# Optimization experiments

Hardware: AMD Instinct MI355X
Metric: run time of the kernel (lower is better)

Reference implementation:

```python
import jax, jax.numpy as jnp
import numpy as np

H_SIZE = 1024
N_HEADS = 16
HEAD_DIM = H_SIZE // N_HEADS
TAU2 = 1.0
LN_EPS = 1e-5


def setup_inputs() -> dict:
    key = jax.random.key(0)
    ks = jax.random.split(key, 12)
    B, S = 2, 1024
    s = 1.0 / np.sqrt(H_SIZE)
    inp = {
        "input": jax.random.normal(ks[0], (B, S, H_SIZE), dtype=jnp.float32),
        "input_mask": jnp.ones((B, S), dtype=jnp.float32),
        # uniform(0,1) noise; converted to Gumbel(0,1) inside reference
        "gumbel": jax.random.uniform(ks[1], (B, N_HEADS, S, S), dtype=jnp.float32,
                                     minval=1e-10, maxval=1.0),
        "Wq": jax.random.normal(ks[2], (H_SIZE, H_SIZE), dtype=jnp.float32) * s,
        "bq": jnp.zeros((H_SIZE,), dtype=jnp.float32),
        "Wk": jax.random.normal(ks[3], (H_SIZE, H_SIZE), dtype=jnp.float32) * s,
        "bk": jnp.zeros((H_SIZE,), dtype=jnp.float32),
        "Wv": jax.random.normal(ks[4], (H_SIZE, H_SIZE), dtype=jnp.float32) * s,
        "bv": jnp.zeros((H_SIZE,), dtype=jnp.float32),
        "Wo": jax.random.normal(ks[5], (H_SIZE, H_SIZE), dtype=jnp.float32) * s,
        "bo": jnp.zeros((H_SIZE,), dtype=jnp.float32),
        "gamma": jnp.ones((H_SIZE,), dtype=jnp.float32),
        "beta": jnp.zeros((H_SIZE,), dtype=jnp.float32),
    }
    return inp


def reference(input, input_mask, gumbel, Wq, bq, Wk, bk, Wv, bv, Wo, bo, gamma, beta):
    B, S, _ = input.shape
    # projections -> [B, H, S, D]
    def proj(W, b):
        y = jnp.einsum('bsh,oh->bso', input, W) + b  # torch Linear: x @ W.T + b
        return y.reshape(B, S, N_HEADS, HEAD_DIM).transpose(0, 2, 1, 3)
    qq = proj(Wq, bq)
    kk = proj(Wk, bk)
    vv = proj(Wv, bv)
    # raw scores (NOTE: original has no 1/sqrt(d) scaling)
    interact = jnp.einsum('bhqd,bhkd->bhqk', qq, kk)
    # gumbel-softmax (soft): softmax((logits + g)/tau)
    g = -jnp.log(-jnp.log(gumbel))
    sto_attn = jax.nn.softmax((interact + g) / TAU2, axis=-1)
    # masking: mask_1 over query dim, mask_2 over key dim
    mask = input_mask[:, None, :, None] * input_mask[:, None, None, :]  # [B,1,S,S]
    attn = sto_attn * mask
    # (dropout p=0 -> identity)
    out = jnp.einsum('bhqk,bhkd->bhqd', attn, vv)
    out = out.transpose(0, 2, 1, 3).reshape(B, S, H_SIZE)
    out = jnp.einsum('bsh,oh->bso', out, Wo) + bo
    # residual + layernorm
    x = out + input
    mu = jnp.mean(x, axis=-1, keepdims=True)
    var = jnp.mean(jnp.square(x - mu), axis=-1, keepdims=True)
    return (x - mu) * jax.lax.rsqrt(var + LN_EPS) * gamma + beta
```

## Files before the change

### kernel.cpp

```cpp
#include <hip/hip_runtime.h>

#define S_LEN 1024
#define HSZ   1024
#define NHEAD 16
#define HD    64
#define BATCH 2
#define MROWS 2048
#define SOFTMAX_M0 50.0f

typedef unsigned short u16;
typedef __attribute__((ext_vector_type(8))) short short8;
typedef __attribute__((ext_vector_type(4))) short short4v;
typedef __attribute__((ext_vector_type(4))) float f32x4;

#define MFMA_BF16(a, b, c) __builtin_amdgcn_mfma_f32_16x16x32_bf16((a), (b), (c), 0, 0, 0)

__device__ __forceinline__ u16 f2bf(float f) {
    union { float f; unsigned u; } c; c.f = f;
    unsigned u = c.u;
    u += 0x7fffu + ((u >> 16) & 1u);
    return (u16)(u >> 16);
}
__device__ __forceinline__ float bf2f(u16 s) {
    union { unsigned u; float f; } c; c.u = ((unsigned)s) << 16;
    return c.f;
}
__device__ __forceinline__ short8 ld8(const u16* p) {
    return *reinterpret_cast<const short8*>(p);
}
__device__ __forceinline__ void gld16(const u16* g, u16* l) {
    __builtin_amdgcn_global_load_lds(
        (const __attribute__((address_space(1))) unsigned int*)g,
        (__attribute__((address_space(3))) unsigned int*)l, 16, 0, 0);
}
__device__ __forceinline__ int frag_off(int row, int cbb) {
    return (((row << 3) | (cbb ^ (row & 7))) << 3);
}

template<int MT>
__device__ __forceinline__ void gemm_tile(const u16* __restrict__ Ag,
                                          const u16* __restrict__ Bg,
                                          int klen, u16* As, u16* Bs,
                                          f32x4 (&acc)[MT][4]) {
    const int tid  = threadIdx.x;
    const int wave = tid >> 6, lane = tid & 63;
    const int lr = lane & 15, grp = lane >> 4;
    const int wm = wave >> 1, wn = wave & 1;

#pragma unroll
    for (int mt = 0; mt < MT; mt++)
#pragma unroll
        for (int nt = 0; nt < 4; nt++)
            acc[mt][nt] = (f32x4){0.f, 0.f, 0.f, 0.f};

    for (int k0 = 0; k0 < klen; k0 += 64) {
        __syncthreads();
#pragma unroll
        for (int j = 0; j < MT; j++) {
            int c = j * 256 + tid, row = c >> 3, cb = (c & 7) ^ (row & 7);
            gld16(Ag + (size_t)row * HSZ + k0 + cb * 8, As + c * 8);
        }
#pragma unroll
        for (int j = 0; j < 4; j++) {
            int c = j * 256 + tid, row = c >> 3, cb = (c & 7) ^ (row & 7);
            gld16(Bg + (size_t)row * HSZ + k0 + cb * 8, Bs + c * 8);
        }
        __syncthreads();

#pragma unroll
        for (int h = 0; h < 2; h++) {
            const int cbb = h * 4 + grp;
            short8 af[MT], bf[4];
#pragma unroll
            for (int mt = 0; mt < MT; mt++)
                af[mt] = ld8(As + frag_off(wm * (MT * 16) + mt * 16 + lr, cbb));
#pragma unroll
            for (int nt = 0; nt < 4; nt++)
                bf[nt] = ld8(Bs + frag_off(wn * 64 + nt * 16 + lr, cbb));
#pragma unroll
            for (int mt = 0; mt < MT; mt++)
#pragma unroll
                for (int nt = 0; nt < 4; nt++)
                    acc[mt][nt] = MFMA_BF16(af[mt], bf[nt], acc[mt][nt]);
        }
    }
}

__global__ __launch_bounds__(256)
void convert_kernel(const float* __restrict__ x,  const float* __restrict__ wq,
                    const float* __restrict__ wk, const float* __restrict__ wv,
                    const float* __restrict__ wo, u16* __restrict__ dst) {
    const int XV = (MROWS * HSZ) / 4;
    const int WV = (HSZ * HSZ) / 4;
    int vid = blockIdx.x * 256 + threadIdx.x;
    const float* src; int off;
    if (vid < XV)            { src = x;  off = vid; }
    else if (vid < XV + WV)  { src = wq; off = vid - XV; }
    else if (vid < XV + 2*WV){ src = wk; off = vid - XV - WV; }
    else if (vid < XV + 3*WV){ src = wv; off = vid - XV - 2*WV; }
    else                     { src = wo; off = vid - XV - 3*WV; }
    float4 v = reinterpret_cast<const float4*>(src)[off];
    ushort4 o;
    o.x = f2bf(v.x); o.y = f2bf(v.y); o.z = f2bf(v.z); o.w = f2bf(v.w);
    reinterpret_cast<ushort4*>(dst)[vid] = o;
}

__global__ __launch_bounds__(256)
void qkv_gemm(const u16* __restrict__ xb,
              const u16* __restrict__ wqb, const u16* __restrict__ wkb,
              const u16* __restrict__ wvb,
              const float* __restrict__ bq, const float* __restrict__ bk,
              const float* __restrict__ bv, const float* __restrict__ mask,
              u16* __restrict__ qout, u16* __restrict__ kout,
              u16* __restrict__ vtout) {
    __shared__ u16 As[64 * 64];
    __shared__ u16 Bs[128 * 64];
    const int ntile = blockIdx.x;
    const int mtile = blockIdx.y;
    const int p  = ntile >> 3;
    const int m0 = mtile * 64;
    const int nw = (ntile & 7) * 128;
    const u16*  W    = (p == 0) ? wqb : (p == 1) ? wkb : wvb;
    const float* bias = (p == 0) ? bq : (p == 1) ? bk : bv;

    f32x4 acc[2][4];
    gemm_tile<2>(xb + (size_t)m0 * HSZ, W + (size_t)nw * HSZ, HSZ, As, Bs, acc);

    const int wave = threadIdx.x >> 6, lane = threadIdx.x & 63;
    const int lr = lane & 15, grp = lane >> 4;
    const int wm = wave >> 1, wn = wave & 1;
#pragma unroll
    for (int mt = 0; mt < 2; mt++)
#pragma unroll
        for (int nt = 0; nt < 4; nt++)
#pragma unroll
            for (int r = 0; r < 4; r++) {
                int m = m0 + wm * 32 + mt * 16 + grp * 4 + r;
                int o = nw + wn * 64 + nt * 16 + lr;
                float val = acc[mt][nt][r] + bias[o];
                int b = m >> 10, s = m & 1023, hh = o >> 6, d = o & 63;
                if (p == 0)
                    qout[(((size_t)(b * NHEAD + hh)) * S_LEN + s) * HD + d] = f2bf(val);
                else if (p == 1)
                    kout[(((size_t)(b * NHEAD + hh)) * S_LEN + s) * HD + d] = f2bf(val);
                else
                    vtout[(((size_t)(b * NHEAD + hh)) * HD + d) * S_LEN + s] =
                        f2bf(val * mask[m]);
            }
}

__global__ __launch_bounds__(256, 4)
void attn_kernel(const u16* __restrict__ qb, const u16* __restrict__ kb,
                 const u16* __restrict__ vt, const float* __restrict__ gumbel,
                 u16* __restrict__ po, float* __restrict__ pl) {
    const int bh   = blockIdx.y;
    const int qt   = blockIdx.x;
    const int half = blockIdx.z;
    const int q0 = qt * 64, kbase = half * 512;
    const int tid = threadIdx.x;
    const int wave = tid >> 6, lane = tid & 63;
    const int lr = lane & 15, grp = lane >> 4;

    const u16* Q = qb + (size_t)bh * S_LEN * HD;
    const u16* K = kb + (size_t)bh * S_LEN * HD;
    const u16* V = vt + (size_t)bh * HD * S_LEN;
    const int qw = q0 + wave * 16;
    const float* Gp = gumbel + (size_t)bh * S_LEN * S_LEN + (size_t)(qw + lr) * S_LEN;

    __shared__ u16 Ks[64 * 64];
    __shared__ u16 Vs[64 * 64];
    __shared__ u16 pbuf[4 * 16 * 68];
    u16* pw = pbuf + wave * (16 * 68);

    short8 aq0 = ld8(Q + (size_t)(qw + lr) * HD + grp * 8);
    short8 aq1 = ld8(Q + (size_t)(qw + lr) * HD + 32 + grp * 8);

    f32x4 acco[4];
#pragma unroll
    for (int i = 0; i < 4; i++) acco[i] = (f32x4){0.f, 0.f, 0.f, 0.f};
    float lsum = 0.f;

    f32x4 gc[4], gn[4];
#pragma unroll
    for (int kt = 0; kt < 4; kt++)
        gc[kt] = *reinterpret_cast<const f32x4*>(Gp + kbase + kt * 16 + grp * 4);

#pragma unroll 1
    for (int it = 0; it < 8; it++) {
        const int k0 = kbase + it * 64;

        __syncthreads();
#pragma unroll
        for (int j = 0; j < 2; j++) {
            int c = j * 256 + tid, row = c >> 3, cb = (c & 7) ^ (row & 7);
            gld16(K + (size_t)(k0 + row) * HD + cb * 8, Ks + c * 8);
        }
#pragma unroll
        for (int j = 0; j < 2; j++) {
            int c = j * 256 + tid, row = c >> 3, cb = (c & 7) ^ (row & 7);
            gld16(V + (size_t)row * S_LEN + k0 + cb * 8, Vs + c * 8);
        }
        __syncthreads();

        if (it < 7) {
#pragma unroll
            for (int kt = 0; kt < 4; kt++)
                gn[kt] = *reinterpret_cast<const f32x4*>(
                             Gp + k0 + 64 + kt * 16 + grp * 4);
        }

#pragma unroll
        for (int kt = 0; kt < 4; kt++) {
            short8 kf0 = ld8(Ks + frag_off(kt * 16 + lr, grp));
            short8 kf1 = ld8(Ks + frag_off(kt * 16 + lr, 4 + grp));
            f32x4 a = (f32x4){0.f, 0.f, 0.f, 0.f};
            a = MFMA_BF16(kf0, aq0, a);
            a = MFMA_BF16(kf1, aq1, a);
            float p[4];
#pragma unroll
            for (int r = 0; r < 4; r++) {
                float w = -__builtin_amdgcn_rcpf(__logf(gc[kt][r]));
                p[r] = __expf(a[r] - SOFTMAX_M0) * w;
                lsum += p[r];
            }
            ushort4 pk;
            pk.x = f2bf(p[0]); pk.y = f2bf(p[1]);
            pk.z = f2bf(p[2]); pk.w = f2bf(p[3]);
            *reinterpret_cast<ushort4*>(pw + lr * 68 + kt * 16 + grp * 4) = pk;
        }

        short8 pa[2];
#pragma unroll
        for (int ks = 0; ks < 2; ks++) {
            const u16* pp = pw + lr * 68 + ks * 32 + grp * 8;
            short4v lo = *reinterpret_cast<const short4v*>(pp);
            short4v hi = *reinterpret_cast<const short4v*>(pp + 4);
            pa[ks] = __builtin_shufflevector(lo, hi, 0, 1, 2, 3, 4, 5, 6, 7);
        }

#pragma unroll
        for (int nt = 0; nt < 4; nt++)
#pragma unroll
            for (int ks = 0; ks < 2; ks++)
                acco[nt] = MFMA_BF16(pa[ks],
                                     ld8(Vs + frag_off(nt * 16 + lr, ks * 4 + grp)),
                                     acco[nt]);

        if (it < 7) {
#pragma unroll
            for (int kt = 0; kt < 4; kt++) gc[kt] = gn[kt];
        }
    }

    lsum += __shfl_xor(lsum, 16, 64);
    lsum += __shfl_xor(lsum, 32, 64);

    const int qbase = ((half * 32 + bh) * 16 + qt) * 64 + wave * 16;
    if (lane < 16) pl[qbase + lane] = lsum;

    const int qidx = qbase + grp * 4;
#pragma unroll
    for (int nt = 0; nt < 4; nt++)
#pragma unroll
        for (int r = 0; r < 4; r++)
            po[(size_t)(qidx + r) * 64 + nt * 16 + lr] = f2bf(acco[nt][r]);
}

__global__ __launch_bounds__(256)
void combine_kernel(const u16* __restrict__ po, const float* __restrict__ pl,
                    const float* __restrict__ mask, u16* __restrict__ ctx) {
    const int qt = blockIdx.x, bh = blockIdx.y;
    const int b = bh >> 4, h = bh & 15;
    const int q = threadIdx.x >> 2;
    const int dc = (threadIdx.x & 3) * 16;
    const int i0 = ((0 * 32 + bh) * 16 + qt) * 64 + q;
    const int i1 = ((1 * 32 + bh) * 16 + qt) * 64 + q;
    float l = pl[i0] + pl[i1];
    float mq = mask[b * S_LEN + qt * 64 + q] / l;
    u16* dst = ctx + ((size_t)(b * S_LEN + qt * 64 + q)) * HSZ + h * 64 + dc;
#pragma unroll
    for (int c = 0; c < 2; c++) {
        short8 a = ld8(po + (size_t)i0 * 64 + dc + c * 8);
        short8 bm = ld8(po + (size_t)i1 * 64 + dc + c * 8);
        short8 o;
#pragma unroll
        for (int j = 0; j < 8; j++)
            o[j] = (short)f2bf((bf2f((u16)a[j]) + bf2f((u16)bm[j])) * mq);
        *reinterpret_cast<short8*>(dst + c * 8) = o;
    }
}

__global__ __launch_bounds__(256)
void oproj_gemm(const u16* __restrict__ A, const u16* __restrict__ W,
                float* __restrict__ part0, float* __restrict__ part1) {
    __shared__ u16 As[64 * 64];
    __shared__ u16 Bs[128 * 64];
    const int ntile = blockIdx.x;
    const int mtile = blockIdx.y;
    const int z     = blockIdx.z;
    const int m0 = mtile * 64, n0 = ntile * 128, koff = z * 512;

    f32x4 acc[2][4];
    gemm_tile<2>(A + (size_t)m0 * HSZ + koff, W + (size_t)n0 * HSZ + koff,
                 512, As, Bs, acc);

    float* dst = z ? part1 : part0;
    const int wave = threadIdx.x >> 6, lane = threadIdx.x & 63;
    const int lr = lane & 15, grp = lane >> 4;
    const int wm = wave >> 1, wn = wave & 1;
#pragma unroll
    for (int mt = 0; mt < 2; mt++)
#pragma unroll
        for (int nt = 0; nt < 4; nt++)
#pragma unroll
            for (int r = 0; r < 4; r++) {
                int m = m0 + wm * 32 + mt * 16 + grp * 4 + r;
                int o = n0 + wn * 64 + nt * 16 + lr;
                dst[(size_t)m * HSZ + o] = acc[mt][nt][r];
            }
}

__global__ __launch_bounds__(256)
void ln_kernel(const float* __restrict__ part0, const float* __restrict__ part1,
               const float* __restrict__ xin, const float* __restrict__ bo,
               const float* __restrict__ gamma, const float* __restrict__ beta,
               float* __restrict__ out) {
    const int row = blockIdx.x;
    const int tid = threadIdx.x;
    const size_t base = (size_t)row * (HSZ / 4);

    float4 p0 = reinterpret_cast<const float4*>(part0)[base + tid];
    float4 p1 = reinterpret_cast<const float4*>(part1)[base + tid];
    float4 xr = reinterpret_cast<const float4*>(xin)[base + tid];
    float4 bb = reinterpret_cast<const float4*>(bo)[tid];
    float4 v;
    v.x = p0.x + p1.x + xr.x + bb.x;
    v.y = p0.y + p1.y + xr.y + bb.y;
    v.z = p0.z + p1.z + xr.z + bb.z;
    v.w = p0.w + p1.w + xr.w + bb.w;

    float s  = v.x + v.y + v.z + v.w;
    float ss = v.x * v.x + v.y * v.y + v.z * v.z + v.w * v.w;
#pragma unroll
    for (int off = 1; off < 64; off <<= 1) {
        s  += __shfl_xor(s, off, 64);
        ss += __shfl_xor(ss, off, 64);
    }
    __shared__ float red[8];
    int wave = tid >> 6, lane = tid & 63;
    if (lane == 0) { red[wave] = s; red[4 + wave] = ss; }
    __syncthreads();
    s  = red[0] + red[1] + red[2] + red[3];
    ss = red[4] + red[5] + red[6] + red[7];
    float mu  = s * (1.f / HSZ);
    float var = ss * (1.f / HSZ) - mu * mu;
    float rstd = rsqrtf(var + 1e-5f);

    float4 g  = reinterpret_cast<const float4*>(gamma)[tid];
    float4 be = reinterpret_cast<const float4*>(beta)[tid];
    float4 o;
    o.x = (v.x - mu) * rstd * g.x + be.x;
    o.y = (v.y - mu) * rstd * g.y + be.y;
    o.z = (v.z - mu) * rstd * g.z + be.z;
    o.w = (v.w - mu) * rstd * g.w + be.w;
    reinterpret_cast<float4*>(out)[base + tid] = o;
}

extern "C" void kernel_launch(void* const* d_in, const int* in_sizes, int n_in,
                              void* d_out, int out_size, void* d_ws, size_t ws_size,
                              hipStream_t stream) {
    (void)in_sizes; (void)n_in; (void)out_size; (void)ws_size;
    const float* x     = (const float*)d_in[0];
    const float* mask  = (const float*)d_in[1];
    const float* gum   = (const float*)d_in[2];
    const float* Wq    = (const float*)d_in[3];
    const float* bq    = (const float*)d_in[4];
    const float* Wk    = (const float*)d_in[5];
    const float* bk    = (const float*)d_in[6];
    const float* Wv    = (const float*)d_in[7];
    const float* bv    = (const float*)d_in[8];
    const float* Wo    = (const float*)d_in[9];
    const float* bo    = (const float*)d_in[10];
    const float* gamma = (const float*)d_in[11];
    const float* beta  = (const float*)d_in[12];
    float* out = (float*)d_out;

    u16* xb  = (u16*)d_ws;
    u16* wqb = xb  + 2097152;
    u16* wkb = wqb + 1048576;
    u16* wvb = wkb + 1048576;
    u16* wob = wvb + 1048576;
    u16* qb  = wob + 1048576;
    u16* kb  = qb  + 2097152;
    u16* vt  = kb  + 2097152;
    u16* ctx = vt  + 2097152;
    float* part0 = (float*)(ctx + 2097152);
    float* pl    = (float*)((char*)part0 + 8388608);
    u16*   po    = xb;
    float* part1 = (float*)xb;

    convert_kernel<<<dim3(6144), dim3(256), 0, stream>>>(x, Wq, Wk, Wv, Wo, xb);
    qkv_gemm<<<dim3(24, 32), dim3(256), 0, stream>>>(xb, wqb, wkb, wvb,
                                                     bq, bk, bv, mask,
                                                     qb, kb, vt);
    attn_kernel<<<dim3(16, 32, 2), dim3(256), 0, stream>>>(qb, kb, vt, gum, po, pl);
    combine_kernel<<<dim3(16, 32), dim3(256), 0, stream>>>(po, pl, mask, ctx);
    oproj_gemm<<<dim3(8, 32, 2), dim3(256), 0, stream>>>(ctx, wob, part0, part1);
    ln_kernel<<<dim3(2048), dim3(256), 0, stream>>>(part0, part1, x, bo,
                                                    gamma, beta, out);
}
```

Baseline: 286.0 us.

## Double-buffer GEMM and attention K tiles, read V fragments directly from global

The shared GEMM tile routine now uses two LDS buffers, so the next k-slice is loaded asynchronously while the current one feeds the MFMAs. This removes one barrier per iteration and hides load latency. The attention kernel double-buffers only K in LDS with a single barrier per step, and loads V fragments straight from global memory into registers instead of staging them in LDS. The cost is doubled LDS in the GEMMs, which may lower occupancy, plus uncoalesced or less cached V reads in attention.

```diff
diff --git a/kernel.cpp b/kernel.cpp
--- a/kernel.cpp
+++ b/kernel.cpp
@@ -46,6 +46,8 @@
     const int wave = tid >> 6, lane = tid & 63;
     const int lr = lane & 15, grp = lane >> 4;
     const int wm = wave >> 1, wn = wave & 1;
+    const int ASZ = MT * 2048;
+    const int BSZ = 8192;
 
 #pragma unroll
     for (int mt = 0; mt < MT; mt++)
@@ -53,19 +55,28 @@
         for (int nt = 0; nt < 4; nt++)
             acc[mt][nt] = (f32x4){0.f, 0.f, 0.f, 0.f};
 
-    for (int k0 = 0; k0 < klen; k0 += 64) {
-        __syncthreads();
+    auto stage = [&](int k0, u16* Ah, u16* Bh) {
 #pragma unroll
         for (int j = 0; j < MT; j++) {
             int c = j * 256 + tid, row = c >> 3, cb = (c & 7) ^ (row & 7);
-            gld16(Ag + (size_t)row * HSZ + k0 + cb * 8, As + c * 8);
+            gld16(Ag + (size_t)row * HSZ + k0 + cb * 8, Ah + c * 8);
         }
 #pragma unroll
         for (int j = 0; j < 4; j++) {
             int c = j * 256 + tid, row = c >> 3, cb = (c & 7) ^ (row & 7);
-            gld16(Bg + (size_t)row * HSZ + k0 + cb * 8, Bs + c * 8);
-        }
+            gld16(Bg + (size_t)row * HSZ + k0 + cb * 8, Bh + c * 8);
+        }
+    };
+
+    stage(0, As, Bs);
+
+    for (int k0 = 0; k0 < klen; k0 += 64) {
+        const int cur = (k0 >> 6) & 1;
+        const u16* Ac = As + cur * ASZ;
+        const u16* Bc = Bs + cur * BSZ;
         __syncthreads();
+        if (k0 + 64 < klen)
+            stage(k0 + 64, As + (cur ^ 1) * ASZ, Bs + (cur ^ 1) * BSZ);
 
 #pragma unroll
         for (int h = 0; h < 2; h++) {
@@ -73,10 +84,10 @@
             short8 af[MT], bf[4];
 #pragma unroll
             for (int mt = 0; mt < MT; mt++)
-                af[mt] = ld8(As + frag_off(wm * (MT * 16) + mt * 16 + lr, cbb));
+                af[mt] = ld8(Ac + frag_off(wm * (MT * 16) + mt * 16 + lr, cbb));
 #pragma unroll
             for (int nt = 0; nt < 4; nt++)
-                bf[nt] = ld8(Bs + frag_off(wn * 64 + nt * 16 + lr, cbb));
+                bf[nt] = ld8(Bc + frag_off(wn * 64 + nt * 16 + lr, cbb));
 #pragma unroll
             for (int mt = 0; mt < MT; mt++)
 #pragma unroll
@@ -113,8 +124,8 @@
               const float* __restrict__ bv, const float* __restrict__ mask,
               u16* __restrict__ qout, u16* __restrict__ kout,
               u16* __restrict__ vtout) {
-    __shared__ u16 As[64 * 64];
-    __shared__ u16 Bs[128 * 64];
+    __shared__ u16 As[2 * 64 * 64];
+    __shared__ u16 Bs[2 * 128 * 64];
     const int ntile = blockIdx.x;
     const int mtile = blockIdx.y;
     const int p  = ntile >> 3;
@@ -167,8 +178,7 @@
     const int qw = q0 + wave * 16;
     const float* Gp = gumbel + (size_t)bh * S_LEN * S_LEN + (size_t)(qw + lr) * S_LEN;
 
-    __shared__ u16 Ks[64 * 64];
-    __shared__ u16 Vs[64 * 64];
+    __shared__ u16 Ks[2][64 * 64];
     __shared__ u16 pbuf[4 * 16 * 68];
     u16* pw = pbuf + wave * (16 * 68);
 
@@ -184,25 +194,24 @@
 #pragma unroll
     for (int kt = 0; kt < 4; kt++)
         gc[kt] = *reinterpret_cast<const f32x4*>(Gp + kbase + kt * 16 + grp * 4);
+
+    auto stageK = [&](int k0, u16* Kh) {
+#pragma unroll
+        for (int j = 0; j < 2; j++) {
+            int c = j * 256 + tid, row = c >> 3, cb = (c & 7) ^ (row & 7);
+            gld16(K + (size_t)(k0 + row) * HD + cb * 8, Kh + c * 8);
+        }
+    };
+    stageK(kbase, Ks[0]);
 
 #pragma unroll 1
     for (int it = 0; it < 8; it++) {
         const int k0 = kbase + it * 64;
+        const int cur = it & 1;
 
         __syncthreads();
-#pragma unroll
-        for (int j = 0; j < 2; j++) {
-            int c = j * 256 + tid, row = c >> 3, cb = (c & 7) ^ (row & 7);
-            gld16(K + (size_t)(k0 + row) * HD + cb * 8, Ks + c * 8);
-        }
-#pragma unroll
-        for (int j = 0; j < 2; j++) {
-            int c = j * 256 + tid, row = c >> 3, cb = (c & 7) ^ (row & 7);
-            gld16(V + (size_t)row * S_LEN + k0 + cb * 8, Vs + c * 8);
-        }
-        __syncthreads();
-
         if (it < 7) {
+            stageK(k0 + 64, Ks[cur ^ 1]);
 #pragma unroll
             for (int kt = 0; kt < 4; kt++)
                 gn[kt] = *reinterpret_cast<const f32x4*>(
@@ -211,8 +220,8 @@
 
 #pragma unroll
         for (int kt = 0; kt < 4; kt++) {
-            short8 kf0 = ld8(Ks + frag_off(kt * 16 + lr, grp));
-            short8 kf1 = ld8(Ks + frag_off(kt * 16 + lr, 4 + grp));
+            short8 kf0 = ld8(Ks[cur] + frag_off(kt * 16 + lr, grp));
+            short8 kf1 = ld8(Ks[cur] + frag_off(kt * 16 + lr, 4 + grp));
             f32x4 a = (f32x4){0.f, 0.f, 0.f, 0.f};
             a = MFMA_BF16(kf0, aq0, a);
             a = MFMA_BF16(kf1, aq1, a);
@@ -239,12 +248,11 @@
         }
 
 #pragma unroll
-        for (int nt = 0; nt < 4; nt++)
-#pragma unroll
-            for (int ks = 0; ks < 2; ks++)
-                acco[nt] = MFMA_BF16(pa[ks],
-                                     ld8(Vs + frag_off(nt * 16 + lr, ks * 4 + grp)),
-                                     acco[nt]);
+        for (int nt = 0; nt < 4; nt++) {
+            const u16* vp = V + (size_t)(nt * 16 + lr) * S_LEN + k0 + grp * 8;
+            acco[nt] = MFMA_BF16(pa[0], ld8(vp), acco[nt]);
+            acco[nt] = MFMA_BF16(pa[1], ld8(vp + 32), acco[nt]);
+        }
 
         if (it < 7) {
 #pragma unroll
@@ -293,8 +301,8 @@
 __global__ __launch_bounds__(256)
 void oproj_gemm(const u16* __restrict__ A, const u16* __restrict__ W,
                 float* __restrict__ part0, float* __restrict__ part1) {
-    __shared__ u16 As[64 * 64];
-    __shared__ u16 Bs[128 * 64];
+    __shared__ u16 As[2 * 64 * 64];
+    __shared__ u16 Bs[2 * 128 * 64];
     const int ntile = blockIdx.x;
     const int mtile = blockIdx.y;
     const int z     = blockIdx.z;
```

Result: slower. 299.0 us (+4.5%).
